# Kernel tuning notes

Hardware: AMD Instinct MI355X
Metric: run time of the kernel (lower is better)

## Reference

```python
import jax, jax.numpy as jnp
import numpy as np

DELTA_V = 0.5
DELTA_D = 3.0
PARAM_VAR = 1.0
PARAM_DIST = 1.0
PARAM_REG = 0.001
NUM_BIN_LABELS = 2   # binary labels in {0,1}
NUM_INST_LABELS = 6  # background + 5 lanes


def _disc_loss_single(pred, labels, num_labels, delta_v, delta_d):
    """pred: [D, N] float, labels: [N] int in [0, num_labels).
    Assumes all labels present (true w.h.p. for large N), so
    torch.unique(sorted=True) == arange(num_labels)."""
    D, N = pred.shape
    K = num_labels
    labels = labels.astype(jnp.int32)
    ones = jnp.ones((N,), dtype=pred.dtype)
    counts = jax.ops.segment_sum(ones, labels, num_segments=K)            # [K]
    sums = jax.ops.segment_sum(pred.T, labels, num_segments=K)            # [K, D]
    means = sums / counts[:, None]                                        # [K, D] segment means

    # variance (pull) term: distance of each pixel embedding to its segment mean
    mu_expand = means[labels]                                             # [N, D]
    dist = jnp.sqrt(jnp.sum((mu_expand - pred.T) ** 2, axis=1))           # [N]
    dist = jnp.maximum(dist - delta_v, 0.0) ** 2
    var_per_label = jax.ops.segment_sum(dist, labels, num_segments=K) / counts
    l_var = jnp.mean(var_per_label)

    # distance (push) term over all ordered pairs i != j of segment means
    diff = means[:, None, :] - means[None, :, :]                          # [K, K, D]
    sq = jnp.sum(diff ** 2, axis=-1)                                      # [K, K]
    offdiag = ~jnp.eye(K, dtype=bool)
    sq_safe = jnp.where(offdiag, sq, 1.0)  # avoid sqrt(0) grad NaN on diagonal
    dn = jnp.maximum(2.0 * delta_d - jnp.sqrt(sq_safe), 0.0) ** 2
    l_dist = jnp.sum(jnp.where(offdiag, dn, 0.0)) / (K * (K - 1))

    # regularizer: mean L2 norm of segment means (norm over feature dim)
    l_reg = jnp.mean(jnp.sqrt(jnp.sum(means ** 2, axis=1)))

    return PARAM_VAR * l_var + PARAM_DIST * l_dist + PARAM_REG * l_reg


def setup_inputs() -> dict:
    key = jax.random.key(0)
    k1, k2, k3, k4 = jax.random.split(key, 4)
    B, MN = 4, 512 * 1024
    return {
        "binary_logits": jax.random.normal(k1, (B, 2, MN), dtype=jnp.float32),
        "binary_labels": jax.random.randint(k2, (B, MN), 0, NUM_BIN_LABELS, dtype=jnp.int64),
        "instance_logits": jax.random.normal(k3, (B, 5, MN), dtype=jnp.float32),
        "instance_labels": jax.random.randint(k4, (B, MN), 0, NUM_INST_LABELS, dtype=jnp.int64),
    }


def reference(binary_logits, binary_labels, instance_logits, instance_labels):
    bin_loss_per = jax.vmap(
        lambda p, l: _disc_loss_single(p, l, NUM_BIN_LABELS, DELTA_V, DELTA_D)
    )(binary_logits, binary_labels)
    inst_loss_per = jax.vmap(
        lambda p, l: _disc_loss_single(p, l, NUM_INST_LABELS, DELTA_V, DELTA_D)
    )(instance_logits, instance_labels)
    return jnp.mean(bin_loss_per), jnp.mean(inst_loss_per)
```

## Files before the change

kernel.cpp:

```cpp
#include <hip/hip_runtime.h>
#include <math.h>

#define DELTA_V 0.5f
#define DELTA_D 3.0f
#define P_REG   0.001f
#define TPB     256
#define NVMAX   36

#define BPSB 64
#define BPSI 128
#define NBLK (4 * BPSB + 4 * BPSI)

#define P1_OFF    0
#define SCAL_OFF  (P1_OFF + NVMAX * NBLK)
#define P2_OFF    (SCAL_OFF + 64)

__device__ __forceinline__ int slice_base(int s) {
    return (s < 4) ? s * BPSB : 4 * BPSB + (s - 4) * BPSI;
}

template<int K, int D>
__device__ void pass1_body(const float* __restrict__ pred,
                           const int*  __restrict__ labels,
                           float* __restrict__ ws,
                           int n4, int bx, int stride, int bid,
                           float (*lredW)[NVMAX]) {
    constexpr int NV = K * (D + 1);
    const float4* pred4 = (const float4*)pred;
    const int4*   lab4  = (const int4*)labels;

    float acc[K][D + 1];
    #pragma unroll
    for (int k = 0; k < K; ++k)
        #pragma unroll
        for (int j = 0; j <= D; ++j) acc[k][j] = 0.f;

    int i = bx * TPB + threadIdx.x;
    bool valid = (i < n4);

    int4   lv;
    float4 xv[D];
    if (valid) {
        lv = lab4[i];
        #pragma unroll
        for (int d = 0; d < D; ++d) xv[d] = pred4[(size_t)d * n4 + i];
    }
    while (valid) {
        const int  inext = i + stride;
        const bool vnext = (inext < n4);
        int4   lvn;
        float4 xvn[D];
        if (vnext) {
            lvn = lab4[inext];
            #pragma unroll
            for (int d = 0; d < D; ++d) xvn[d] = pred4[(size_t)d * n4 + inext];
        }

        int labs[4] = {lv.x, lv.y, lv.z, lv.w};
        const float* xs = (const float*)&xv[0];
        #pragma unroll
        for (int c = 0; c < 4; ++c) {
            const int lab = labs[c];
            #pragma unroll
            for (int k = 0; k < K; ++k) {
                const float ind = (lab == k) ? 1.f : 0.f;
                acc[k][D] += ind;
                #pragma unroll
                for (int d = 0; d < D; ++d)
                    acc[k][d] = fmaf(ind, xs[d * 4 + c], acc[k][d]);
            }
        }

        i = inext; valid = vnext;
        lv = lvn;
        #pragma unroll
        for (int d = 0; d < D; ++d) xv[d] = xvn[d];
    }

    const int wave = threadIdx.x >> 6, lane = threadIdx.x & 63;
    #pragma unroll
    for (int k = 0; k < K; ++k) {
        #pragma unroll
        for (int j = 0; j <= D; ++j) {
            float v = acc[k][j];
            for (int off = 32; off > 0; off >>= 1) v += __shfl_down(v, off);
            if (lane == 0) lredW[wave][k * (D + 1) + j] = v;
        }
    }
    __syncthreads();
    if (threadIdx.x < NV) {
        const int t = threadIdx.x;
        ws[P1_OFF + (size_t)t * NBLK + bid] =
            lredW[0][t] + lredW[1][t] + lredW[2][t] + lredW[3][t];
    }
}

__global__ __launch_bounds__(TPB)
void pass1_k(const float* __restrict__ bl, const int* __restrict__ bL,
             const float* __restrict__ il, const int* __restrict__ iL,
             float* __restrict__ ws, int MN) {
    __shared__ float lredW[4][NVMAX];
    const int bid = blockIdx.x, n4 = MN >> 2;
    if (bid < 4 * BPSB) {
        const int s = bid / BPSB, bx = bid - s * BPSB;
        pass1_body<2, 2>(bl + (size_t)s * 2 * MN, bL + (size_t)s * MN,
                         ws, n4, bx, BPSB * TPB, bid, lredW);
    } else {
        const int r = bid - 4 * BPSB;
        const int si = r / BPSI, bx = r - si * BPSI;
        pass1_body<6, 5>(il + (size_t)si * 5 * MN, iL + (size_t)si * MN,
                         ws, n4, bx, BPSI * TPB, bid, lredW);
    }
}

template<int K, int D, int NBP>
__device__ void pass2_slice(const float* __restrict__ pred,
                            const int*  __restrict__ labels,
                            float* __restrict__ ws,
                            const int s, const int bx, const int bid, const int n4) {
    constexpr int NV = K * (D + 1);
    __shared__ float tot[NVMAX];
    __shared__ float muS[30];
    __shared__ float cntS[6];
    __shared__ float lredW[4][6];
    const int t = threadIdx.x;
    const int sliceBase = bid - bx;

    if (t < NV) {
        const float* P = ws + P1_OFF + (size_t)t * NBLK + sliceBase;
        float v = 0.f;
        #pragma unroll 8
        for (int j = 0; j < NBP; ++j) v += P[j];
        tot[t] = v;
        const int k = t / (D + 1), jj = t - k * (D + 1);
        if (jj == D) cntS[k] = v;
    }
    __syncthreads();
    if (t < NV) {
        const int k = t / (D + 1), jj = t - k * (D + 1);
        if (jj < D) muS[k * D + jj] = tot[t] / cntS[k];
    }
    __syncthreads();

    if (bx == 0) {
        if (t < K) ws[SCAL_OFF + s * 8 + t] = cntS[t];
        if (t == 0) {
            float l_dist = 0.f, l_reg = 0.f;
            for (int i = 0; i < K; ++i) {
                float n2 = 0.f;
                for (int d = 0; d < D; ++d) n2 += muS[i * D + d] * muS[i * D + d];
                l_reg += sqrtf(n2);
                for (int j = 0; j < K; ++j) {
                    if (i == j) continue;
                    float sq = 0.f;
                    for (int d = 0; d < D; ++d) {
                        const float df = muS[i * D + d] - muS[j * D + d];
                        sq += df * df;
                    }
                    const float dn = fmaxf(2.f * DELTA_D - sqrtf(sq), 0.f);
                    l_dist += dn * dn;
                }
            }
            ws[SCAL_OFF + s * 8 + 6] =
                l_dist / (float)(K * (K - 1)) + P_REG * (l_reg / (float)K);
        }
    }

    const float4* pred4 = (const float4*)pred;
    const int4*   lab4  = (const int4*)labels;

    float acc[K];
    #pragma unroll
    for (int k = 0; k < K; ++k) acc[k] = 0.f;

    const int stride = NBP * TPB;
    int i = bx * TPB + t;
    bool valid = (i < n4);
    int4   lv;
    float4 xv[D];
    if (valid) {
        lv = lab4[i];
        #pragma unroll
        for (int d = 0; d < D; ++d) xv[d] = pred4[(size_t)d * n4 + i];
    }
    while (valid) {
        const int  inext = i + stride;
        const bool vnext = (inext < n4);
        int4   lvn;
        float4 xvn[D];
        if (vnext) {
            lvn = lab4[inext];
            #pragma unroll
            for (int d = 0; d < D; ++d) xvn[d] = pred4[(size_t)d * n4 + inext];
        }

        int labs[4] = {lv.x, lv.y, lv.z, lv.w};
        const float* xs = (const float*)&xv[0];
        #pragma unroll
        for (int c = 0; c < 4; ++c) {
            const int lab = labs[c];
            float sq = 0.f;
            #pragma unroll
            for (int d = 0; d < D; ++d) {
                const float df = muS[lab * D + d] - xs[d * 4 + c];
                sq = fmaf(df, df, sq);
            }
            const float h = fmaxf(sqrtf(sq) - DELTA_V, 0.f);
            const float h2 = h * h;
            #pragma unroll
            for (int k = 0; k < K; ++k)
                acc[k] += (lab == k) ? h2 : 0.f;
        }

        i = inext; valid = vnext;
        lv = lvn;
        #pragma unroll
        for (int d = 0; d < D; ++d) xv[d] = xvn[d];
    }

    const int wave = t >> 6, lane = t & 63;
    #pragma unroll
    for (int k = 0; k < K; ++k) {
        float v = acc[k];
        for (int off = 32; off > 0; off >>= 1) v += __shfl_down(v, off);
        if (lane == 0) lredW[wave][k] = v;
    }
    __syncthreads();
    if (t < K)
        ws[P2_OFF + (size_t)bid * 6 + t] =
            lredW[0][t] + lredW[1][t] + lredW[2][t] + lredW[3][t];
}

__global__ __launch_bounds__(TPB)
void pass2_k(const float* __restrict__ bl, const int* __restrict__ bL,
             const float* __restrict__ il, const int* __restrict__ iL,
             float* __restrict__ ws, int MN) {
    const int bid = blockIdx.x, n4 = MN >> 2;
    if (bid < 4 * BPSB) {
        const int s = bid / BPSB, bx = bid - s * BPSB;
        pass2_slice<2, 2, BPSB>(bl + (size_t)s * 2 * MN, bL + (size_t)s * MN,
                                ws, s, bx, bid, n4);
    } else {
        const int r = bid - 4 * BPSB;
        const int si = r / BPSI, bx = r - si * BPSI;
        pass2_slice<6, 5, BPSI>(il + (size_t)si * 5 * MN, iL + (size_t)si * MN,
                                ws, 4 + si, bx, bid, n4);
    }
}

__global__ void final_k(const float* __restrict__ ws, float* __restrict__ out) {
    __shared__ float contrib[48];
    const int t = threadIdx.x;
    if (t < 48) {
        const int s = t / 6, k = t - (t / 6) * 6;
        const int Ks = (s < 4) ? 2 : 6;
        const int NB = (s < 4) ? BPSB : BPSI;
        const int base = slice_base(s);
        float c = 0.f;
        if (k < Ks) {
            float v = 0.f;
            for (int j = 0; j < NB; ++j)
                v += ws[P2_OFF + (size_t)(base + j) * 6 + k];
            c = v / ws[SCAL_OFF + s * 8 + k];
        }
        contrib[t] = c;
    }
    __syncthreads();
    if (t == 0) {
        float totB = 0.f, totI = 0.f;
        for (int s = 0; s < 8; ++s) {
            const int Ks = (s < 4) ? 2 : 6;
            float lv = 0.f;
            for (int k = 0; k < Ks; ++k) lv += contrib[s * 6 + k];
            lv /= (float)Ks;
            const float loss = lv + ws[SCAL_OFF + s * 8 + 6];
            if (s < 4) totB += loss; else totI += loss;
        }
        out[0] = totB * 0.25f;
        out[1] = totI * 0.25f;
    }
}

extern "C" void kernel_launch(void* const* d_in, const int* in_sizes, int n_in,
                              void* d_out, int out_size, void* d_ws, size_t ws_size,
                              hipStream_t stream) {
    const float* bl = (const float*)d_in[0];
    const int*   bL = (const int*)d_in[1];
    const float* il = (const float*)d_in[2];
    const int*   iL = (const int*)d_in[3];
    float* ws  = (float*)d_ws;
    float* out = (float*)d_out;

    const int B  = 4;
    const int MN = in_sizes[1] / B;

    pass1_k<<<dim3(NBLK), dim3(TPB), 0, stream>>>(bl, bL, il, iL, ws, MN);
    pass2_k<<<dim3(NBLK), dim3(TPB), 0, stream>>>(bl, bL, il, iL, ws, MN);
    final_k<<<dim3(1), dim3(64), 0, stream>>>(ws, out);
}
```

Before: 139.4 us.

## Pack labels to bytes in pass one and reuse them in pass two

Pass one now writes each label as a byte into a workspace buffer, and pass two reads those packed bytes instead of the 32-bit labels, cutting its label traffic by four. Block counts per slice are doubled, the manual software prefetch is replaced with a plain strided loop, and the pass-two partials are transposed so the final reduction reads contiguously. The byte buffer is sized from a hard-coded pixel count and adds extra writes in pass one.

```diff
diff --git a/kernel.cpp b/kernel.cpp
--- a/kernel.cpp
+++ b/kernel.cpp
@@ -7,12 +7,13 @@
 #define TPB     256
 #define NVMAX   36
 
-#define BPSB 64
-#define BPSI 128
+#define BPSB 128
+#define BPSI 256
 #define NBLK (4 * BPSB + 4 * BPSI)
 
 #define P1_OFF    0
-#define SCAL_OFF  (P1_OFF + NVMAX * NBLK)
+#define LBL_OFF   (P1_OFF + NVMAX * NBLK)
+#define SCAL_OFF  (LBL_OFF + 2 * 524288)
 #define P2_OFF    (SCAL_OFF + 64)
 
 __device__ __forceinline__ int slice_base(int s) {
@@ -23,6 +24,7 @@
 __device__ void pass1_body(const float* __restrict__ pred,
                            const int*  __restrict__ labels,
                            float* __restrict__ ws,
+                           uchar4* __restrict__ lblPack,
                            int n4, int bx, int stride, int bid,
                            float (*lredW)[NVMAX]) {
     constexpr int NV = K * (D + 1);
@@ -35,28 +37,14 @@
         #pragma unroll
         for (int j = 0; j <= D; ++j) acc[k][j] = 0.f;
 
-    int i = bx * TPB + threadIdx.x;
-    bool valid = (i < n4);
-
-    int4   lv;
-    float4 xv[D];
-    if (valid) {
-        lv = lab4[i];
+    for (int i = bx * TPB + threadIdx.x; i < n4; i += stride) {
+        int4 lv = lab4[i];
+        int labs[4] = {lv.x, lv.y, lv.z, lv.w};
+        lblPack[i] = make_uchar4((unsigned char)lv.x, (unsigned char)lv.y,
+                                 (unsigned char)lv.z, (unsigned char)lv.w);
+        float4 xv[D];
         #pragma unroll
         for (int d = 0; d < D; ++d) xv[d] = pred4[(size_t)d * n4 + i];
-    }
-    while (valid) {
-        const int  inext = i + stride;
-        const bool vnext = (inext < n4);
-        int4   lvn;
-        float4 xvn[D];
-        if (vnext) {
-            lvn = lab4[inext];
-            #pragma unroll
-            for (int d = 0; d < D; ++d) xvn[d] = pred4[(size_t)d * n4 + inext];
-        }
-
-        int labs[4] = {lv.x, lv.y, lv.z, lv.w};
         const float* xs = (const float*)&xv[0];
         #pragma unroll
         for (int c = 0; c < 4; ++c) {
@@ -70,11 +58,6 @@
                     acc[k][d] = fmaf(ind, xs[d * 4 + c], acc[k][d]);
             }
         }
-
-        i = inext; valid = vnext;
-        lv = lvn;
-        #pragma unroll
-        for (int d = 0; d < D; ++d) xv[d] = xvn[d];
     }
 
     const int wave = threadIdx.x >> 6, lane = threadIdx.x & 63;
@@ -101,21 +84,22 @@
              float* __restrict__ ws, int MN) {
     __shared__ float lredW[4][NVMAX];
     const int bid = blockIdx.x, n4 = MN >> 2;
+    uchar4* lblBase = (uchar4*)(ws + LBL_OFF);
     if (bid < 4 * BPSB) {
         const int s = bid / BPSB, bx = bid - s * BPSB;
         pass1_body<2, 2>(bl + (size_t)s * 2 * MN, bL + (size_t)s * MN,
-                         ws, n4, bx, BPSB * TPB, bid, lredW);
+                         ws, lblBase + (size_t)s * n4, n4, bx, BPSB * TPB, bid, lredW);
     } else {
         const int r = bid - 4 * BPSB;
         const int si = r / BPSI, bx = r - si * BPSI;
         pass1_body<6, 5>(il + (size_t)si * 5 * MN, iL + (size_t)si * MN,
-                         ws, n4, bx, BPSI * TPB, bid, lredW);
+                         ws, lblBase + (size_t)(4 + si) * n4, n4, bx, BPSI * TPB, bid, lredW);
     }
 }
 
 template<int K, int D, int NBP>
 __device__ void pass2_slice(const float* __restrict__ pred,
-                            const int*  __restrict__ labels,
+                            const uchar4* __restrict__ lblPack,
                             float* __restrict__ ws,
                             const int s, const int bx, const int bid, const int n4) {
     constexpr int NV = K * (D + 1);
@@ -167,34 +151,18 @@
     }
 
     const float4* pred4 = (const float4*)pred;
-    const int4*   lab4  = (const int4*)labels;
 
     float acc[K];
     #pragma unroll
     for (int k = 0; k < K; ++k) acc[k] = 0.f;
 
     const int stride = NBP * TPB;
-    int i = bx * TPB + t;
-    bool valid = (i < n4);
-    int4   lv;
-    float4 xv[D];
-    if (valid) {
-        lv = lab4[i];
+    for (int i = bx * TPB + t; i < n4; i += stride) {
+        const uchar4 lq = lblPack[i];
+        int labs[4] = {lq.x, lq.y, lq.z, lq.w};
+        float4 xv[D];
         #pragma unroll
         for (int d = 0; d < D; ++d) xv[d] = pred4[(size_t)d * n4 + i];
-    }
-    while (valid) {
-        const int  inext = i + stride;
-        const bool vnext = (inext < n4);
-        int4   lvn;
-        float4 xvn[D];
-        if (vnext) {
-            lvn = lab4[inext];
-            #pragma unroll
-            for (int d = 0; d < D; ++d) xvn[d] = pred4[(size_t)d * n4 + inext];
-        }
-
-        int labs[4] = {lv.x, lv.y, lv.z, lv.w};
         const float* xs = (const float*)&xv[0];
         #pragma unroll
         for (int c = 0; c < 4; ++c) {
@@ -211,11 +179,6 @@
             for (int k = 0; k < K; ++k)
                 acc[k] += (lab == k) ? h2 : 0.f;
         }
-
-        i = inext; valid = vnext;
-        lv = lvn;
-        #pragma unroll
-        for (int d = 0; d < D; ++d) xv[d] = xvn[d];
     }
 
     const int wave = t >> 6, lane = t & 63;
@@ -227,23 +190,23 @@
     }
     __syncthreads();
     if (t < K)
-        ws[P2_OFF + (size_t)bid * 6 + t] =
+        ws[P2_OFF + (size_t)t * NBLK + bid] =
             lredW[0][t] + lredW[1][t] + lredW[2][t] + lredW[3][t];
 }
 
 __global__ __launch_bounds__(TPB)
-void pass2_k(const float* __restrict__ bl, const int* __restrict__ bL,
-             const float* __restrict__ il, const int* __restrict__ iL,
+void pass2_k(const float* __restrict__ bl, const float* __restrict__ il,
              float* __restrict__ ws, int MN) {
     const int bid = blockIdx.x, n4 = MN >> 2;
+    const uchar4* lblBase = (const uchar4*)(ws + LBL_OFF);
     if (bid < 4 * BPSB) {
         const int s = bid / BPSB, bx = bid - s * BPSB;
-        pass2_slice<2, 2, BPSB>(bl + (size_t)s * 2 * MN, bL + (size_t)s * MN,
+        pass2_slice<2, 2, BPSB>(bl + (size_t)s * 2 * MN, lblBase + (size_t)s * n4,
                                 ws, s, bx, bid, n4);
     } else {
         const int r = bid - 4 * BPSB;
         const int si = r / BPSI, bx = r - si * BPSI;
-        pass2_slice<6, 5, BPSI>(il + (size_t)si * 5 * MN, iL + (size_t)si * MN,
+        pass2_slice<6, 5, BPSI>(il + (size_t)si * 5 * MN, lblBase + (size_t)(4 + si) * n4,
                                 ws, 4 + si, bx, bid, n4);
     }
 }
@@ -258,9 +221,10 @@
         const int base = slice_base(s);
         float c = 0.f;
         if (k < Ks) {
+            const float* P = ws + P2_OFF + (size_t)k * NBLK + base;
             float v = 0.f;
-            for (int j = 0; j < NB; ++j)
-                v += ws[P2_OFF + (size_t)(base + j) * 6 + k];
+            #pragma unroll 8
+            for (int j = 0; j < NB; ++j) v += P[j];
             c = v / ws[SCAL_OFF + s * 8 + k];
         }
         contrib[t] = c;
@@ -295,6 +259,6 @@
     const int MN = in_sizes[1] / B;
 
     pass1_k<<<dim3(NBLK), dim3(TPB), 0, stream>>>(bl, bL, il, iL, ws, MN);
-    pass2_k<<<dim3(NBLK), dim3(TPB), 0, stream>>>(bl, bL, il, iL, ws, MN);
+    pass2_k<<<dim3(NBLK), dim3(TPB), 0, stream>>>(bl, il, ws, MN);
     final_k<<<dim3(1), dim3(64), 0, stream>>>(ws, out);
 }
```

Result: faster. 135.8 us (median of 2 runs) (-2.6%).
